# Optimization experiments

Hardware: AMD Instinct MI355X
Metric: run time of the kernel (lower is better)

Reference implementation:

```python
import jax, jax.numpy as jnp
import numpy as np

N_VERTS = 100000
N_FACES = 200000
C = 512


def setup_inputs() -> dict:
    key = jax.random.key(0)
    ks = jax.random.split(key, 12)
    x = jax.random.normal(ks[0], (1, N_VERTS, C), dtype=jnp.float32) * 0.1
    verts = jax.random.normal(ks[1], (N_VERTS, 3), dtype=jnp.float32)
    faces = jax.random.randint(ks[2], (N_FACES, 3), 0, N_VERTS, dtype=jnp.int32)
    def lin(k, fan_in, fan_out):
        return jax.random.normal(k, (fan_in, fan_out), dtype=jnp.float32) / np.sqrt(fan_in)
    return {
        "x": x, "verts": verts, "faces": faces,
        "W1": lin(ks[3], C, C),    "b1": jnp.zeros((C,), jnp.float32),
        "W2": lin(ks[4], C, 512),  "b2": jnp.zeros((512,), jnp.float32),
        "W3": lin(ks[5], 512, 256),"b3": jnp.zeros((256,), jnp.float32),
        "W4": lin(ks[6], 256, 12), "b4": jnp.zeros((12,), jnp.float32),
    }


def special_procrustes(M):
    # roma.special_procrustes: nearest rotation in SO(3) to M, batched [F,3,3]
    U, S, Vh = jnp.linalg.svd(M)
    det = jnp.linalg.det(jnp.matmul(U, Vh))  # [F]
    D = jnp.stack([jnp.ones_like(det), jnp.ones_like(det), det], axis=-1)  # [F,3]
    return jnp.matmul(U * D[:, None, :], Vh)


def reference(x, verts, faces, W1, b1, W2, b2, W3, b3, W4, b4):
    N = verts.shape[0]
    F = faces.shape[0]
    # prism base: gather 3 vertex positions per face -> [F,3,3]
    prism_base = verts[faces]
    # gather features of the 3 face vertices and mean over them -> [F,C]
    feat = x[0][faces].mean(axis=1)
    # mlp_refine
    h = jax.nn.relu(feat @ W1 + b1)
    h = jax.nn.relu(h @ W2 + b2)
    h = jax.nn.relu(h @ W3 + b3)
    out = h @ W4 + b4  # [F,12]
    # batched 3x3 Procrustes rotation + translation
    rotations = special_procrustes(out[:, :9].reshape(F, 3, 3))
    translations = out[:, 9:]  # [F,3]
    transformed_prism = jnp.matmul(prism_base, rotations) + translations[:, None, :]  # [F,3,3]
    # scatter-add back to vertices with per-vertex face-count normalization
    flat_idx = faces.reshape(-1)  # [3F]
    summed = jax.ops.segment_sum(transformed_prism.reshape(-1, 3), flat_idx, num_segments=N)
    counts = jax.ops.segment_sum(jnp.ones((3 * F,), jnp.float32), flat_idx, num_segments=N)
    features = summed / jnp.clip(counts, 1.0)[:, None]  # [N,3]
    return features[None], transformed_prism, rotations
```

## Files before the change

### kernel.cpp

```cpp
#include <hip/hip_runtime.h>
#include <hip/hip_bf16.h>
#include <stdint.h>

typedef __attribute__((ext_vector_type(8))) short short8;
typedef __attribute__((ext_vector_type(4))) float f32x4;
typedef __attribute__((ext_vector_type(4))) unsigned short u16x4;

__device__ __forceinline__ float bf2f(unsigned short h) {
    union { uint32_t u; float f; } v; v.u = ((uint32_t)h) << 16;
    return v.f;
}
__device__ __forceinline__ void split_rne(float f, unsigned short& hi, unsigned short& lo) {
    __hip_bfloat16 h = __float2bfloat16(f);
    union { __hip_bfloat16 b; unsigned short u; } ch; ch.b = h; hi = ch.u;
    float hf = __bfloat162float(h);
    __hip_bfloat16 l = __float2bfloat16(f - hf);
    union { __hip_bfloat16 b; unsigned short u; } cl; cl.b = l; lo = cl.u;
}
__device__ __forceinline__ void splitT(float f, unsigned short& hi, unsigned short& lo) {
    union { float f; uint32_t u; } a; a.f = f;
    hi = (unsigned short)(a.u >> 16);
    union { uint32_t u; float f; } b; b.u = a.u & 0xFFFF0000u;
    union { float f; uint32_t u; } c; c.f = f - b.f;
    lo = (unsigned short)(c.u >> 16);
}

__device__ __forceinline__ void gld_lds16(const void* g, void* s) {
    __builtin_amdgcn_global_load_lds(
        (const __attribute__((address_space(1))) void*)(uintptr_t)g,
        (__attribute__((address_space(3))) void*)(uint32_t)(uintptr_t)s,
        16, 0, 0);
}

__device__ __forceinline__ f32x4 mfma16(short8 a, short8 b, f32x4 c) {
    return __builtin_amdgcn_mfma_f32_16x16x32_bf16(a, b, c, 0, 0, 0);
}

__global__ void prep_weights(const float* __restrict__ W1, const float* __restrict__ W2,
                             const float* __restrict__ W3,
                             unsigned short* __restrict__ w1h, unsigned short* __restrict__ w1l,
                             unsigned short* __restrict__ w2h, unsigned short* __restrict__ w2l,
                             unsigned short* __restrict__ w3h, unsigned short* __restrict__ w3l,
                             float* __restrict__ sums, float* __restrict__ counts, int nverts) {
    int t = blockIdx.x * 256 + threadIdx.x;
    if (t < nverts * 3) sums[t] = 0.0f;
    if (t < nverts)     counts[t] = 0.0f;
    float v; unsigned short *ph, *pl; size_t o;
    if (t < 262144) {
        int k = t >> 9, n = t & 511;
        v = W1[t]; o = (size_t)n * 512 + k; ph = w1h; pl = w1l;
    } else if (t < 524288) {
        int u = t - 262144; int k = u >> 9, n = u & 511;
        v = W2[u]; o = (size_t)n * 512 + k; ph = w2h; pl = w2l;
    } else if (t < 655360) {
        int u = t - 524288; int k = u >> 8, n = u & 255;
        v = W3[u]; o = (size_t)n * 512 + k; ph = w3h; pl = w3l;
    } else return;
    unsigned short hi, lo;
    split_rne(v, hi, lo);
    ph[o] = hi; pl[o] = lo;
}

__global__ void gather_mean(const float* __restrict__ x, const int* __restrict__ faces,
                            unsigned short* __restrict__ Fhi, unsigned short* __restrict__ Flo,
                            int fbase, int fcount, int mrows) {
    int t = blockIdx.x * 256 + threadIdx.x;
    if (t >= (mrows << 7)) return;
    int r = t >> 7;
    int c = (t & 127) << 2;
    f32x4 m = {0.f, 0.f, 0.f, 0.f};
    if (r < fcount) {
        int f = fbase + r;
        int i0 = faces[3 * f], i1 = faces[3 * f + 1], i2 = faces[3 * f + 2];
        f32x4 a = *(const f32x4*)(x + (size_t)i0 * 512 + c);
        f32x4 b = *(const f32x4*)(x + (size_t)i1 * 512 + c);
        f32x4 d = *(const f32x4*)(x + (size_t)i2 * 512 + c);
        m = (a + b + d) * (1.0f / 3.0f);
    }
    u16x4 hv, lv;
#pragma unroll
    for (int j = 0; j < 4; ++j) {
        unsigned short hi, lo;
        split_rne(m[j], hi, lo);
        hv[j] = hi; lv[j] = lo;
    }
    *(u16x4*)(Fhi + (size_t)r * 512 + c) = hv;
    *(u16x4*)(Flo + (size_t)r * 512 + c) = lv;
}

template<int OUT>
__global__ __launch_bounds__(256, 2)
void gemm_pipe(const unsigned short* __restrict__ Ahi, const unsigned short* __restrict__ Alo,
               const unsigned short* __restrict__ Bhi, const unsigned short* __restrict__ Blo,
               const float* __restrict__ bias,
               void* __restrict__ Out0, unsigned short* __restrict__ Olo,
               int N, int K, int nt) {
    __shared__ __align__(16) unsigned short sm[2][4][128 * 32];

    const int tid  = threadIdx.x;
    const int lane = tid & 63;
    const int w    = tid >> 6;
    const int wr = w >> 1, wc = w & 1;

    const int nwg  = gridDim.x;
    const int orig = blockIdx.x;
    const int q = nwg >> 3, r8 = nwg & 7;
    const int xcd = orig & 7, idx = orig >> 3;
    const int wg = (xcd < r8 ? xcd * (q + 1) : r8 * (q + 1) + (xcd - r8) * q) + idx;
    const int m0 = (wg / nt) << 7;
    const int n0 = (wg % nt) << 7;

    f32x4 acc[4][4] = {};

    const int s_lo  = w * 64 + lane;
    const int row0  = s_lo >> 2;
    const int c0    = ((s_lo & 3) - ((row0 >> 1) & 3)) & 3;
    const int s_hi  = 256 + s_lo;
    const int row1  = (s_hi >> 2) & 127;
    const int c1    = ((s_hi & 3) - ((row1 >> 1) & 3)) & 3;

    const uint32_t oA0 = (uint32_t)(m0 + row0) * (uint32_t)K + (c0 << 3);
    const uint32_t oA1 = (uint32_t)(m0 + row1) * (uint32_t)K + (c1 << 3);
    const uint32_t oB0 = (uint32_t)(n0 + row0) * (uint32_t)K + (c0 << 3);
    const uint32_t oB1 = (uint32_t)(n0 + row1) * (uint32_t)K + (c1 << 3);

    auto stage = [&](int b, int t) {
        const uint32_t k0 = t << 5;
        gld_lds16(Ahi + oA0 + k0, &sm[b][0][(w * 64) * 8]);
        gld_lds16(Ahi + oA1 + k0, &sm[b][0][(256 + w * 64) * 8]);
        gld_lds16(Alo + oA0 + k0, &sm[b][1][(w * 64) * 8]);
        gld_lds16(Alo + oA1 + k0, &sm[b][1][(256 + w * 64) * 8]);
        gld_lds16(Bhi + oB0 + k0, &sm[b][2][(w * 64) * 8]);
        gld_lds16(Bhi + oB1 + k0, &sm[b][2][(256 + w * 64) * 8]);
        gld_lds16(Blo + oB0 + k0, &sm[b][3][(w * 64) * 8]);
        gld_lds16(Blo + oB1 + k0, &sm[b][3][(256 + w * 64) * 8]);
    };

    const int NT = K >> 5;
    stage(0, 0);
    stage(1, 1);

    const int kc  = lane >> 4;
    const int rbA = (wr << 6) + (lane & 15);
    const int rbB = (wc << 6) + (lane & 15);

    for (int t = 0; t < NT; ++t) {
        const int cur = t & 1;

        if (t + 1 < NT) asm volatile("s_waitcnt vmcnt(8)" ::: "memory");
        else            asm volatile("s_waitcnt vmcnt(0)" ::: "memory");
        __builtin_amdgcn_s_barrier();

        short8 ah[4], al[4], bh[4], bl[4];
#pragma unroll
        for (int m = 0; m < 4; ++m) {
            const int r   = rbA + (m << 4);
            const int off = r * 32 + (((kc + (r >> 1)) & 3) << 3);
            ah[m] = *(const short8*)&sm[cur][0][off];
            al[m] = *(const short8*)&sm[cur][1][off];
        }
#pragma unroll
        for (int n = 0; n < 4; ++n) {
            const int r   = rbB + (n << 4);
            const int off = r * 32 + (((kc + (r >> 1)) & 3) << 3);
            bh[n] = *(const short8*)&sm[cur][2][off];
            bl[n] = *(const short8*)&sm[cur][3][off];
        }
        asm volatile("s_waitcnt lgkmcnt(0)" ::: "memory");
        __builtin_amdgcn_sched_barrier(0);
        __builtin_amdgcn_s_barrier();

        if (t + 2 < NT) stage(cur, t + 2);

        __builtin_amdgcn_s_setprio(1);
#pragma unroll
        for (int m = 0; m < 4; ++m)
#pragma unroll
            for (int n = 0; n < 4; ++n)
                acc[m][n] = mfma16(ah[m], bh[n], acc[m][n]);
#pragma unroll
        for (int m = 0; m < 4; ++m)
#pragma unroll
            for (int n = 0; n < 4; ++n)
                acc[m][n] = mfma16(al[m], bh[n], acc[m][n]);
#pragma unroll
        for (int m = 0; m < 4; ++m)
#pragma unroll
            for (int n = 0; n < 4; ++n)
                acc[m][n] = mfma16(ah[m], bl[n], acc[m][n]);
        __builtin_amdgcn_s_setprio(0);
    }

#pragma unroll
    for (int n = 0; n < 4; ++n) {
        const int col = n0 + (wc << 6) + (n << 4) + (lane & 15);
        const float bv = (OUT == 1) ? 0.0f : bias[col];
#pragma unroll
        for (int m = 0; m < 4; ++m) {
            const int rbase = m0 + (wr << 6) + (m << 4) + ((lane >> 4) << 2);
#pragma unroll
            for (int j = 0; j < 4; ++j) {
                const size_t o = (size_t)(rbase + j) * N + col;
                if (OUT == 1) {
                    ((float*)Out0)[o] = acc[m][n][j];
                } else if (OUT == 2) {
                    ((float*)Out0)[o] = fmaxf(acc[m][n][j] + bv, 0.0f);
                } else {
                    float v = fmaxf(acc[m][n][j] + bv, 0.0f);
                    unsigned short hi, lo;
                    split_rne(v, hi, lo);
                    ((unsigned short*)Out0)[o] = hi;
                    Olo[o] = lo;
                }
            }
        }
    }
}

__global__ __launch_bounds__(256, 2)
void gemm_l1(const float* __restrict__ X,
             const unsigned short* __restrict__ Bhi, const unsigned short* __restrict__ Blo,
             float* __restrict__ Out,
             int N, int K, int nt, int nvalid) {
    __shared__ __align__(16) unsigned short sm[2][4][128 * 32];

    const int tid  = threadIdx.x;
    const int lane = tid & 63;
    const int w    = tid >> 6;
    const int wr = w >> 1, wc = w & 1;

    const int nwg  = gridDim.x;
    const int orig = blockIdx.x;
    const int q = nwg >> 3, r8 = nwg & 7;
    const int xcd = orig & 7, idx = orig >> 3;
    const int wg = (xcd < r8 ? xcd * (q + 1) : r8 * (q + 1) + (xcd - r8) * q) + idx;
    const int m0 = (wg / nt) << 7;
    const int n0 = (wg % nt) << 7;

    f32x4 acc[4][4] = {};

    int adst[2], avalid[2];
    uint32_t xoff[2];
#pragma unroll
    for (int i = 0; i < 2; ++i) {
        const int s   = i * 256 + tid;
        const int row = s >> 2;
        const int c   = s & 3;
        adst[i]   = row * 32 + (((c + (row >> 1)) & 3) << 3);
        avalid[i] = (m0 + row) < nvalid;
        xoff[i]   = (uint32_t)(avalid[i] ? (m0 + row) : 0) * (uint32_t)K + (c << 3);
    }
    const int s_lo  = w * 64 + lane;
    const int row0  = s_lo >> 2;
    const int c0    = ((s_lo & 3) - ((row0 >> 1) & 3)) & 3;
    const int s_hi  = 256 + s_lo;
    const int row1  = (s_hi >> 2) & 127;
    const int c1    = ((s_hi & 3) - ((row1 >> 1) & 3)) & 3;
    const uint32_t oB0 = (uint32_t)(n0 + row0) * (uint32_t)K + (c0 << 3);
    const uint32_t oB1 = (uint32_t)(n0 + row1) * (uint32_t)K + (c1 << 3);

    f32x4 fA[2][2];

    auto issueA = [&](int t) {
        const uint32_t k0 = t << 5;
#pragma unroll
        for (int i = 0; i < 2; ++i) {
            const float* src = X + xoff[i] + k0;
            fA[i][0] = *(const f32x4*)src;
            fA[i][1] = *(const f32x4*)(src + 4);
        }
    };
    auto issueB = [&](int b, int t) {
        const uint32_t k0 = t << 5;
        gld_lds16(Bhi + oB0 + k0, &sm[b][2][(w * 64) * 8]);
        gld_lds16(Bhi + oB1 + k0, &sm[b][2][(256 + w * 64) * 8]);
        gld_lds16(Blo + oB0 + k0, &sm[b][3][(w * 64) * 8]);
        gld_lds16(Blo + oB1 + k0, &sm[b][3][(256 + w * 64) * 8]);
    };
    auto cvtWriteA = [&](int b) {
#pragma unroll
        for (int i = 0; i < 2; ++i) {
            short8 hv, lv;
#pragma unroll
            for (int j = 0; j < 8; ++j) {
                float f = avalid[i] ? fA[i][j >> 2][j & 3] : 0.0f;
                unsigned short hi, lo;
                splitT(f, hi, lo);
                hv[j] = (short)hi;
                lv[j] = (short)lo;
            }
            *(short8*)&sm[b][0][adst[i]] = hv;
            *(short8*)&sm[b][1][adst[i]] = lv;
        }
    };

    const int NT = K >> 5;
    issueA(0); issueB(0, 0);
    asm volatile("s_waitcnt vmcnt(4)" ::: "memory");
    cvtWriteA(0);
    issueA(1); issueB(1, 1);
    asm volatile("s_waitcnt vmcnt(4)" ::: "memory");
    cvtWriteA(1);
    asm volatile("s_waitcnt lgkmcnt(0)" ::: "memory");

    const int kc  = lane >> 4;
    const int rbA = (wr << 6) + (lane & 15);
    const int rbB = (wc << 6) + (lane & 15);

    for (int t = 0; t < NT; ++t) {
        const int cur = t & 1;

        if (t + 1 < NT) asm volatile("s_waitcnt vmcnt(4)" ::: "memory");
        else            asm volatile("s_waitcnt vmcnt(0)" ::: "memory");
        __builtin_amdgcn_s_barrier();

        if (t + 2 < NT) issueA(t + 2);

        short8 ah[4], al[4], bh[4], bl[4];
#pragma unroll
        for (int m = 0; m < 4; ++m) {
            const int r   = rbA + (m << 4);
            const int off = r * 32 + (((kc + (r >> 1)) & 3) << 3);
            ah[m] = *(const short8*)&sm[cur][0][off];
            al[m] = *(const short8*)&sm[cur][1][off];
        }
#pragma unroll
        for (int n = 0; n < 4; ++n) {
            const int r   = rbB + (n << 4);
            const int off = r * 32 + (((kc + (r >> 1)) & 3) << 3);
            bh[n] = *(const short8*)&sm[cur][2][off];
            bl[n] = *(const short8*)&sm[cur][3][off];
        }
        asm volatile("s_waitcnt lgkmcnt(0)" ::: "memory");
        __builtin_amdgcn_sched_barrier(0);
        __builtin_amdgcn_s_barrier();

        if (t + 2 < NT) issueB(cur, t + 2);

        __builtin_amdgcn_s_setprio(1);
#pragma unroll
        for (int m = 0; m < 4; ++m)
#pragma unroll
            for (int n = 0; n < 4; ++n)
                acc[m][n] = mfma16(ah[m], bh[n], acc[m][n]);
#pragma unroll
        for (int m = 0; m < 4; ++m)
#pragma unroll
            for (int n = 0; n < 4; ++n)
                acc[m][n] = mfma16(al[m], bh[n], acc[m][n]);
#pragma unroll
        for (int m = 0; m < 4; ++m)
#pragma unroll
            for (int n = 0; n < 4; ++n)
                acc[m][n] = mfma16(ah[m], bl[n], acc[m][n]);
        __builtin_amdgcn_s_setprio(0);

        if (t + 2 < NT) {
            asm volatile("s_waitcnt vmcnt(4)" ::: "memory");
            cvtWriteA(cur);
        }
    }

#pragma unroll
    for (int n = 0; n < 4; ++n) {
        const int col = n0 + (wc << 6) + (n << 4) + (lane & 15);
#pragma unroll
        for (int m = 0; m < 4; ++m) {
            const int rbase = m0 + (wr << 6) + (m << 4) + ((lane >> 4) << 2);
#pragma unroll
            for (int j = 0; j < 4; ++j)
                Out[(size_t)(rbase + j) * N + col] = acc[m][n][j];
        }
    }
}

__global__ __launch_bounds__(256, 2)
void gemm_l2w(const float* __restrict__ Y, const int* __restrict__ faces,
              const float* __restrict__ b1,
              const unsigned short* __restrict__ Bhi, const unsigned short* __restrict__ Blo,
              const float* __restrict__ bias2,
              unsigned short* __restrict__ Ohi, unsigned short* __restrict__ Olo,
              int K, int nvalid) {
    __shared__ __align__(16) unsigned short sm[2][2][64 * 32];

    const int tid  = threadIdx.x;
    const int lane = tid & 63;
    const int w    = tid >> 6;

    const int nwg  = gridDim.x;
    const int orig = blockIdx.x;
    const int q = nwg >> 3, r8 = nwg & 7;
    const int xcd = orig & 7, idx = orig >> 3;
    const int wg = (xcd < r8 ? xcd * (q + 1) : r8 * (q + 1) + (xcd - r8) * q) + idx;
    const int m0 = wg << 6;

    f32x4 acc[4][8] = {};

    const int arow = tid >> 2;
    const int achk = tid & 3;
    const int adst = arow * 32 + (((achk + (arow >> 1)) & 3) << 3);
    const int gf   = m0 + arow;
    const int avalid = gf < nvalid;
    const int gfs  = avalid ? gf : 0;
    uint32_t yoff[3];
#pragma unroll
    for (int r = 0; r < 3; ++r)
        yoff[r] = (uint32_t)faces[3 * gfs + r] * (uint32_t)K;

    const uint32_t bBase = (uint32_t)((w << 7) + (lane & 15)) * (uint32_t)K + ((lane >> 4) << 3);

    f32x4 fA[3][2];
    f32x4 fb[2];

    auto issueA = [&](int t) {
        const uint32_t koff = (uint32_t)(t << 5) + (achk << 3);
#pragma unroll
        for (int r = 0; r < 3; ++r) {
            const float* src = Y + yoff[r] + koff;
            fA[r][0] = *(const f32x4*)src;
            fA[r][1] = *(const f32x4*)(src + 4);
        }
        fb[0] = *(const f32x4*)(b1 + koff);
        fb[1] = *(const f32x4*)(b1 + koff + 4);
    };
    auto cvtWriteA = [&](int b) {
        short8 hv, lv;
#pragma unroll
        for (int j = 0; j < 8; ++j) {
            const int h = j >> 2, e = j & 3;
            float f = 0.0f;
            if (avalid) {
                f = fmaf(fA[0][h][e] + fA[1][h][e] + fA[2][h][e], 1.0f / 3.0f, fb[h][e]);
                f = fmaxf(f, 0.0f);
            }
            unsigned short hi, lo;
            splitT(f, hi, lo);
            hv[j] = (short)hi;
            lv[j] = (short)lo;
        }
        *(short8*)&sm[b][0][adst] = hv;
        *(short8*)&sm[b][1][adst] = lv;
    };

    const int NT = K >> 5;
    issueA(0); cvtWriteA(0);
    issueA(1); cvtWriteA(1);
    asm volatile("s_waitcnt lgkmcnt(0)" ::: "memory");
    __builtin_amdgcn_s_barrier();

    const int kc  = lane >> 4;
    const int rlA = lane & 15;

    for (int t = 0; t < NT; ++t) {
        const int cur = t & 1;
        const uint32_t k0 = (uint32_t)(t << 5);

        if (t + 2 < NT) issueA(t + 2);

        short8 bh[4], bl[4];
#pragma unroll
        for (int n = 0; n < 4; ++n) {
            bh[n] = *(const short8*)(Bhi + bBase + (uint32_t)(n * 16) * (uint32_t)K + k0);
            bl[n] = *(const short8*)(Blo + bBase + (uint32_t)(n * 16) * (uint32_t)K + k0);
        }

        short8 ah[4], al[4];
#pragma unroll
        for (int m = 0; m < 4; ++m) {
            const int r   = rlA + (m << 4);
            const int off = r * 32 + (((kc + (r >> 1)) & 3) << 3);
            ah[m] = *(const short8*)&sm[cur][0][off];
            al[m] = *(const short8*)&sm[cur][1][off];
        }
        asm volatile("s_waitcnt lgkmcnt(0)" ::: "memory");
        __builtin_amdgcn_sched_barrier(0);
        __builtin_amdgcn_s_barrier();

        __builtin_amdgcn_s_setprio(1);
#pragma unroll
        for (int m = 0; m < 4; ++m)
#pragma unroll
            for (int n = 0; n < 4; ++n)
                acc[m][n] = mfma16(ah[m], bh[n], acc[m][n]);
#pragma unroll
        for (int m = 0; m < 4; ++m)
#pragma unroll
            for (int n = 0; n < 4; ++n)
                acc[m][n] = mfma16(al[m], bh[n], acc[m][n]);
#pragma unroll
        for (int m = 0; m < 4; ++m)
#pragma unroll
            for (int n = 0; n < 4; ++n)
                acc[m][n] = mfma16(ah[m], bl[n], acc[m][n]);
        __builtin_amdgcn_s_setprio(0);

#pragma unroll
        for (int n = 0; n < 4; ++n) {
            bh[n] = *(const short8*)(Bhi + bBase + (uint32_t)((n + 4) * 16) * (uint32_t)K + k0);
            bl[n] = *(const short8*)(Blo + bBase + (uint32_t)((n + 4) * 16) * (uint32_t)K + k0);
        }
        __builtin_amdgcn_s_setprio(1);
#pragma unroll
        for (int m = 0; m < 4; ++m)
#pragma unroll
            for (int n = 0; n < 4; ++n)
                acc[m][4 + n] = mfma16(ah[m], bh[n], acc[m][4 + n]);
#pragma unroll
        for (int m = 0; m < 4; ++m)
#pragma unroll
            for (int n = 0; n < 4; ++n)
                acc[m][4 + n] = mfma16(al[m], bh[n], acc[m][4 + n]);
#pragma unroll
        for (int m = 0; m < 4; ++m)
#pragma unroll
            for (int n = 0; n < 4; ++n)
                acc[m][4 + n] = mfma16(ah[m], bl[n], acc[m][4 + n]);
        __builtin_amdgcn_s_setprio(0);

        if (t + 2 < NT) cvtWriteA(cur);
    }

#pragma unroll
    for (int n = 0; n < 8; ++n) {
        const int col = (w << 7) + (n << 4) + (lane & 15);
        const float bv = bias2[col];
#pragma unroll
        for (int m = 0; m < 4; ++m) {
            const int rbase = m0 + (m << 4) + ((lane >> 4) << 2);
#pragma unroll
            for (int j = 0; j < 4; ++j) {
                const size_t o = (size_t)(rbase + j) * 512 + col;
                float v = fmaxf(acc[m][n][j] + bv, 0.0f);
                unsigned short hi, lo;
                split_rne(v, hi, lo);
                Ohi[o] = hi;
                Olo[o] = lo;
            }
        }
    }
}

#define JROT(app, aqq, apq, apz, aqz, vp0, vp1, vp2, vq0, vq1, vq2) do {          \
    float _apq = (apq);                                                            \
    if (fabsf(_apq) > 1e-30f) {                                                    \
        float _tau = ((aqq) - (app)) / (2.0f * _apq);                              \
        float _t = copysignf(1.0f, _tau) / (fabsf(_tau) + sqrtf(1.0f + _tau*_tau));\
        float _c = 1.0f / sqrtf(1.0f + _t*_t);                                     \
        float _s = _t * _c;                                                        \
        (app) = (app) - _t * _apq;                                                 \
        (aqq) = (aqq) + _t * _apq;                                                 \
        (apq) = 0.0f;                                                              \
        float _pz = (apz), _qz = (aqz);                                            \
        (apz) = _c * _pz - _s * _qz;                                               \
        (aqz) = _s * _pz + _c * _qz;                                               \
        float _x;                                                                  \
        _x = (vp0); (vp0) = _c*_x - _s*(vq0); (vq0) = _s*_x + _c*(vq0);            \
        _x = (vp1); (vp1) = _c*_x - _s*(vq1); (vq1) = _s*_x + _c*(vq1);            \
        _x = (vp2); (vp2) = _c*_x - _s*(vq2); (vq2) = _s*_x + _c*(vq2);            \
    }                                                                              \
} while (0)

#define SWAP3(la, lb, x0, y0, z0, x1, y1, z1) do {                \
    float _tm;                                                    \
    _tm = la; la = lb; lb = _tm;                                  \
    _tm = x0; x0 = x1; x1 = _tm;                                  \
    _tm = y0; y0 = y1; y1 = _tm;                                  \
    _tm = z0; z0 = z1; z1 = _tm;                                  \
} while (0)

__global__ void face_kernel(const float* __restrict__ H3,
                            const float* __restrict__ W4, const float* __restrict__ b4,
                            const float* __restrict__ verts, const int* __restrict__ faces,
                            float* __restrict__ out_tp, float* __restrict__ out_rot,
                            float* __restrict__ sums, float* __restrict__ counts,
                            int fbase, int fcount) {
    __shared__ float sW[256 * 12 + 12];
    for (int i = threadIdx.x; i < 256 * 12 + 12; i += 256)
        sW[i] = (i < 256 * 12) ? W4[i] : b4[i - 256 * 12];
    __syncthreads();

    const int r = blockIdx.x * 256 + threadIdx.x;
    if (r >= fcount) return;
    const int f = fbase + r;

    float o[12];
#pragma unroll
    for (int n = 0; n < 12; ++n) o[n] = sW[3072 + n];
    const f32x4* ph = (const f32x4*)(H3 + (size_t)r * 256);
    for (int kb = 0; kb < 64; ++kb) {
        f32x4 hv = ph[kb];
#pragma unroll
        for (int kk = 0; kk < 4; ++kk) {
            float val = hv[kk];
            const float* wrow = &sW[(kb * 4 + kk) * 12];
#pragma unroll
            for (int n = 0; n < 12; ++n) o[n] = fmaf(val, wrow[n], o[n]);
        }
    }

    const float M00=o[0], M01=o[1], M02=o[2];
    const float M10=o[3], M11=o[4], M12=o[5];
    const float M20=o[6], M21=o[7], M22=o[8];
    const float t0 =o[9], t1 =o[10], t2 =o[11];

    float a00 = M00*M00 + M10*M10 + M20*M20;
    float a11 = M01*M01 + M11*M11 + M21*M21;
    float a22 = M02*M02 + M12*M12 + M22*M22;
    float a01 = M00*M01 + M10*M11 + M20*M21;
    float a02 = M00*M02 + M10*M12 + M20*M22;
    float a12 = M01*M02 + M11*M12 + M21*M22;

    float v00=1.f, v01=0.f, v02=0.f;
    float v10=0.f, v11=1.f, v12=0.f;
    float v20=0.f, v21=0.f, v22=1.f;
#pragma unroll
    for (int sweep = 0; sweep < 5; ++sweep) {
        JROT(a00, a11, a01, a02, a12, v00, v10, v20, v01, v11, v21);
        JROT(a00, a22, a02, a01, a12, v00, v10, v20, v02, v12, v22);
        JROT(a11, a22, a12, a01, a02, v01, v11, v21, v02, v12, v22);
    }
    float l0 = a00, l1 = a11, l2 = a22;
    if (l0 < l1) SWAP3(l0, l1, v00, v10, v20, v01, v11, v21);
    if (l0 < l2) SWAP3(l0, l2, v00, v10, v20, v02, v12, v22);
    if (l1 < l2) SWAP3(l1, l2, v01, v11, v21, v02, v12, v22);

    float b1x = M00*v00 + M01*v10 + M02*v20;
    float b1y = M10*v00 + M11*v10 + M12*v20;
    float b1z = M20*v00 + M21*v10 + M22*v20;
    float b2x = M00*v01 + M01*v11 + M02*v21;
    float b2y = M10*v01 + M11*v11 + M12*v21;
    float b2z = M20*v01 + M21*v11 + M22*v21;

    float n1 = sqrtf(b1x*b1x + b1y*b1y + b1z*b1z);
    float u1x, u1y, u1z;
    if (n1 > 1e-25f) { float in = 1.0f / n1; u1x = b1x*in; u1y = b1y*in; u1z = b1z*in; }
    else             { u1x = 1.f; u1y = 0.f; u1z = 0.f; }

    float dp  = b2x*u1x + b2y*u1y + b2z*u1z;
    float w2x = b2x - dp*u1x, w2y = b2y - dp*u1y, w2z = b2z - dp*u1z;
    float n2  = sqrtf(w2x*w2x + w2y*w2y + w2z*w2z);
    float u2x, u2y, u2z;
    if (n2 > 1e-25f) { float in = 1.0f / n2; u2x = w2x*in; u2y = w2y*in; u2z = w2z*in; }
    else {
        float ex = (fabsf(u1x) < 0.9f) ? 1.f : 0.f;
        float ey = 1.f - ex;
        float cx = -u1z * ey, cy = u1z * ex, cz = u1x * ey - u1y * ex;
        float cn = rsqrtf(cx*cx + cy*cy + cz*cz);
        u2x = cx * cn; u2y = cy * cn; u2z = cz * cn;
    }
    float u3x = u1y*u2z - u1z*u2y;
    float u3y = u1z*u2x - u1x*u2z;
    float u3z = u1x*u2y - u1y*u2x;

    float dv = v00*(v11*v22 - v12*v21) - v01*(v10*v22 - v12*v20) + v02*(v10*v21 - v11*v20);
    if (dv < 0.f) { v02 = -v02; v12 = -v12; v22 = -v22; }

    float R00 = u1x*v00 + u2x*v01 + u3x*v02;
    float R01 = u1x*v10 + u2x*v11 + u3x*v12;
    float R02 = u1x*v20 + u2x*v21 + u3x*v22;
    float R10 = u1y*v00 + u2y*v01 + u3y*v02;
    float R11 = u1y*v10 + u2y*v11 + u3y*v12;
    float R12 = u1y*v20 + u2y*v21 + u3y*v22;
    float R20 = u1z*v00 + u2z*v01 + u3z*v02;
    float R21 = u1z*v10 + u2z*v11 + u3z*v12;
    float R22 = u1z*v20 + u2z*v21 + u3z*v22;

    float* rp = out_rot + (size_t)f * 9;
    rp[0]=R00; rp[1]=R01; rp[2]=R02;
    rp[3]=R10; rp[4]=R11; rp[5]=R12;
    rp[6]=R20; rp[7]=R21; rp[8]=R22;

    float* tp = out_tp + (size_t)f * 9;
    const int idx[3] = { faces[3*f], faces[3*f+1], faces[3*f+2] };
#pragma unroll
    for (int j = 0; j < 3; ++j) {
        const int vi = idx[j];
        float px = verts[3*vi], py = verts[3*vi+1], pz = verts[3*vi+2];
        float q0 = px*R00 + py*R10 + pz*R20 + t0;
        float q1 = px*R01 + py*R11 + pz*R21 + t1;
        float q2 = px*R02 + py*R12 + pz*R22 + t2;
        tp[j*3+0] = q0; tp[j*3+1] = q1; tp[j*3+2] = q2;
        atomicAdd(&sums[(size_t)vi*3+0], q0);
        atomicAdd(&sums[(size_t)vi*3+1], q1);
        atomicAdd(&sums[(size_t)vi*3+2], q2);
        atomicAdd(&counts[vi], 1.0f);
    }
}

__global__ void finalize_kernel(float* __restrict__ feats, const float* __restrict__ counts, int nverts) {
    int v = blockIdx.x * 256 + threadIdx.x;
    if (v >= nverts) return;
    float c = fmaxf(counts[v], 1.0f);
    feats[v*3+0] = feats[v*3+0] / c;
    feats[v*3+1] = feats[v*3+1] / c;
    feats[v*3+2] = feats[v*3+2] / c;
}

extern "C" void kernel_launch(void* const* d_in, const int* in_sizes, int n_in,
                              void* d_out, int out_size, void* d_ws, size_t ws_size,
                              hipStream_t stream) {
    const float* x     = (const float*)d_in[0];
    const float* verts = (const float*)d_in[1];
    const int*   faces = (const int*)d_in[2];
    const float* W1 = (const float*)d_in[3];
    const float* b1 = (const float*)d_in[4];
    const float* W2 = (const float*)d_in[5];
    const float* b2 = (const float*)d_in[6];
    const float* W3 = (const float*)d_in[7];
    const float* b3 = (const float*)d_in[8];
    const float* W4 = (const float*)d_in[9];
    const float* b4 = (const float*)d_in[10];

    const int nverts = in_sizes[1] / 3;
    const int nfaces = in_sizes[2] / 3;

    float* out_feats = (float*)d_out;
    float* out_tp    = out_feats + (size_t)nverts * 3;
    float* out_rot   = out_tp + (size_t)nfaces * 9;

    char* ws = (char*)d_ws;
    size_t cur = 0;
    auto carve = [&](size_t bytes) -> void* {
        void* p = ws + cur;
        cur += (bytes + 255) & ~(size_t)255;
        return p;
    };
    unsigned short* w1h = (unsigned short*)carve(512 * 512 * 2);
    unsigned short* w1l = (unsigned short*)carve(512 * 512 * 2);
    unsigned short* w2h = (unsigned short*)carve(512 * 512 * 2);
    unsigned short* w2l = (unsigned short*)carve(512 * 512 * 2);
    unsigned short* w3h = (unsigned short*)carve(256 * 512 * 2);
    unsigned short* w3l = (unsigned short*)carve(256 * 512 * 2);
    float* counts = (float*)carve((size_t)nverts * 4);

    const long MV = ((long)nverts + 127) & ~127L;
    const long MF = ((long)nfaces + 127) & ~127L;
    const size_t szY   = (size_t)MV * 512 * 4;
    const size_t szH2w = (size_t)MF * 512 * 2;
    const size_t szH3f = (size_t)MF * 256 * 4;

    const size_t sR1 = (szY > szH3f) ? szY : szH3f;
    const size_t sR2 = szH2w;
    const size_t sR3 = szH2w;
    const size_t need = cur + sR1 + sR2 + sR3 + 4 * 256;

    prep_weights<<<(655360 + 255) / 256, 256, 0, stream>>>(W1, W2, W3, w1h, w1l, w2h, w2l, w3h, w3l,
                                                           out_feats, counts, nverts);

    if (ws_size >= need) {
        char* R1 = (char*)carve(sR1);
        char* R2 = (char*)carve(sR2);
        char* R3 = (char*)carve(sR3);
        float*          y   = (float*)R1;
        float*          h3  = (float*)R1;
        unsigned short* h2h = (unsigned short*)R2;
        unsigned short* h2l = (unsigned short*)R3;

        gemm_l1<<<(int)(MV / 128) * 4, 256, 0, stream>>>(x, w1h, w1l, y, 512, 512, 4, nverts);

        gemm_l2w<<<(int)(MF / 64), 256, 0, stream>>>(y, faces, b1, w2h, w2l, b2,
                                                     h2h, h2l, 512, nfaces);

        gemm_pipe<2><<<(int)(MF / 128) * 2, 256, 0, stream>>>(h2h, h2l, w3h, w3l, b3, h3, nullptr, 256, 512, 2);

        face_kernel<<<(nfaces + 255) / 256, 256, 0, stream>>>(h3, W4, b4, verts, faces,
                                                              out_tp, out_rot, out_feats, counts,
                                                              0, nfaces);
    } else {
        long mpad = MF;
        size_t avail = (ws_size > cur) ? (ws_size - cur) : 0;
        long chp = (long)(avail / 4096);
        chp &= ~127L;
        if (chp > mpad) chp = mpad;
        if (chp < 128) chp = 128;
        unsigned short* bAh = (unsigned short*)carve((size_t)chp * 512 * 2);
        unsigned short* bAl = (unsigned short*)carve((size_t)chp * 512 * 2);
        unsigned short* bBh = (unsigned short*)carve((size_t)chp * 512 * 2);
        unsigned short* bBl = (unsigned short*)carve((size_t)chp * 512 * 2);

        for (long base = 0; base < nfaces; base += chp) {
            long rem = (long)nfaces - base;
            int cnt = (int)((rem < chp) ? rem : chp);
            int mc  = (cnt + 127) & ~127;

            gather_mean<<<mc / 2, 256, 0, stream>>>(x, faces, bAh, bAl, (int)base, cnt, mc);
            gemm_pipe<0><<<(mc / 128) * 4, 256, 0, stream>>>(bAh, bAl, w1h, w1l, b1, bBh, bBl, 512, 512, 4);
            gemm_pipe<0><<<(mc / 128) * 4, 256, 0, stream>>>(bBh, bBl, w2h, w2l, b2, bAh, bAl, 512, 512, 4);
            gemm_pipe<2><<<(mc / 128) * 2, 256, 0, stream>>>(bAh, bAl, w3h, w3l, b3, (float*)bBh, nullptr, 256, 512, 2);
            face_kernel<<<(cnt + 255) / 256, 256, 0, stream>>>((float*)bBh, W4, b4, verts, faces,
                                                               out_tp, out_rot, out_feats, counts,
                                                               (int)base, cnt);
        }
    }

    finalize_kernel<<<(nverts + 255) / 256, 256, 0, stream>>>(out_feats, counts, nverts);
}
```

Measured before the change: 1.182 ms.

## Retile layer-2 gather GEMM to 128x256 tiles with LDS-staged B

Replaces the 64-row, full-width layer-2 GEMM (4 waves, each streaming its B columns directly from global memory) with a 512-thread kernel using 128x256 output tiles across a 2x4 wave grid. The B operand (hi/lo split weights) is now loaded asynchronously into shared memory with swizzled direct-to-LDS loads, so each B fragment is shared across waves instead of being re-read per wave. The A-side gather, mean, bias and ReLU fusion is kept. The change aims to cut redundant global and L2 traffic for the weights and raise MFMA reuse. In exchange the gathered A rows are now loaded twice (once per N half) and there is more barrier synchronization per K step.

```diff
diff --git a/kernel.cpp b/kernel.cpp
--- a/kernel.cpp
+++ b/kernel.cpp
@@ -374,27 +374,30 @@
     }
 }
 
-__global__ __launch_bounds__(256, 2)
-void gemm_l2w(const float* __restrict__ Y, const int* __restrict__ faces,
+__global__ __launch_bounds__(512, 2)
+void gemm_l2n(const float* __restrict__ Y, const int* __restrict__ faces,
               const float* __restrict__ b1,
               const unsigned short* __restrict__ Bhi, const unsigned short* __restrict__ Blo,
               const float* __restrict__ bias2,
               unsigned short* __restrict__ Ohi, unsigned short* __restrict__ Olo,
               int K, int nvalid) {
-    __shared__ __align__(16) unsigned short sm[2][2][64 * 32];
+    __shared__ __align__(16) unsigned short smA[2][2][128 * 32];
+    __shared__ __align__(16) unsigned short smB[2][256 * 32];
 
     const int tid  = threadIdx.x;
     const int lane = tid & 63;
     const int w    = tid >> 6;
+    const int wr = w >> 2, wc = w & 3;
 
     const int nwg  = gridDim.x;
     const int orig = blockIdx.x;
     const int q = nwg >> 3, r8 = nwg & 7;
     const int xcd = orig & 7, idx = orig >> 3;
     const int wg = (xcd < r8 ? xcd * (q + 1) : r8 * (q + 1) + (xcd - r8) * q) + idx;
-    const int m0 = wg << 6;
-
-    f32x4 acc[4][8] = {};
+    const int m0 = (wg >> 1) << 7;
+    const int n0 = (wg & 1) << 8;
+
+    f32x4 acc[4][4] = {};
 
     const int arow = tid >> 2;
     const int achk = tid & 3;
@@ -407,7 +410,12 @@
     for (int r = 0; r < 3; ++r)
         yoff[r] = (uint32_t)faces[3 * gfs + r] * (uint32_t)K;
 
-    const uint32_t bBase = (uint32_t)((w << 7) + (lane & 15)) * (uint32_t)K + ((lane >> 4) << 3);
+    const int brow0 = tid >> 2;
+    const int bc0   = ((tid & 3) - ((brow0 >> 1) & 3)) & 3;
+    const int brow1 = 128 + brow0;
+    const int bc1   = ((tid & 3) - ((brow1 >> 1) & 3)) & 3;
+    const uint32_t oB0 = (uint32_t)(n0 + brow0) * (uint32_t)K + (bc0 << 3);
+    const uint32_t oB1 = (uint32_t)(n0 + brow1) * (uint32_t)K + (bc1 << 3);
 
     f32x4 fA[3][2];
     f32x4 fb[2];
@@ -422,6 +430,13 @@
         }
         fb[0] = *(const f32x4*)(b1 + koff);
         fb[1] = *(const f32x4*)(b1 + koff + 4);
+    };
+    auto issueB = [&](int t) {
+        const uint32_t k0 = t << 5;
+        gld_lds16(Bhi + oB0 + k0, &smB[0][(w * 64) * 8]);
+        gld_lds16(Bhi + oB1 + k0, &smB[0][(512 + w * 64) * 8]);
+        gld_lds16(Blo + oB0 + k0, &smB[1][(w * 64) * 8]);
+        gld_lds16(Blo + oB1 + k0, &smB[1][(512 + w * 64) * 8]);
     };
     auto cvtWriteA = [&](int b) {
         short8 hv, lv;
@@ -438,44 +453,52 @@
             hv[j] = (short)hi;
             lv[j] = (short)lo;
         }
-        *(short8*)&sm[b][0][adst] = hv;
-        *(short8*)&sm[b][1][adst] = lv;
+        *(short8*)&smA[b][0][adst] = hv;
+        *(short8*)&smA[b][1][adst] = lv;
     };
 
     const int NT = K >> 5;
-    issueA(0); cvtWriteA(0);
-    issueA(1); cvtWriteA(1);
+    issueA(0); issueB(0);
+    asm volatile("s_waitcnt vmcnt(4)" ::: "memory");
+    cvtWriteA(0);
+    issueA(1);
+    asm volatile("s_waitcnt vmcnt(0)" ::: "memory");
+    cvtWriteA(1);
     asm volatile("s_waitcnt lgkmcnt(0)" ::: "memory");
-    __builtin_amdgcn_s_barrier();
-
-    const int kc  = lane >> 4;
-    const int rlA = lane & 15;
+
+    const int kc = lane >> 4;
+    const int rA = (wr << 6) + (lane & 15);
+    const int rB = (wc << 6) + (lane & 15);
 
     for (int t = 0; t < NT; ++t) {
         const int cur = t & 1;
-        const uint32_t k0 = (uint32_t)(t << 5);
+
+        asm volatile("s_waitcnt vmcnt(0)" ::: "memory");
+        __builtin_amdgcn_s_barrier();
 
         if (t + 2 < NT) issueA(t + 2);
 
-        short8 bh[4], bl[4];
+        short8 ah[4], al[4], bh[4], bl[4];
+#pragma unroll
+        for (int m = 0; m < 4; ++m) {
+            const int r   = rA + (m << 4);
+            const int off = r * 32 + (((kc + (r >> 1)) & 3) << 3);
+            ah[m] = *(const short8*)&smA[cur][0][off];
+            al[m] = *(const short8*)&smA[cur][1][off];
+        }
 #pragma unroll
         for (int n = 0; n < 4; ++n) {
-            bh[n] = *(const short8*)(Bhi + bBase + (uint32_t)(n * 16) * (uint32_t)K + k0);
-            bl[n] = *(const short8*)(Blo + bBase + (uint32_t)(n * 16) * (uint32_t)K + k0);
-        }
-
-        short8 ah[4], al[4];
-#pragma unroll
-        for (int m = 0; m < 4; ++m) {
-            const int r   = rlA + (m << 4);
+            const int r   = rB + (n << 4);
             const int off = r * 32 + (((kc + (r >> 1)) & 3) << 3);
-            ah[m] = *(const short8*)&sm[cur][0][off];
-            al[m] = *(const short8*)&sm[cur][1][off];
+            bh[n] = *(const short8*)&smB[0][off];
+            bl[n] = *(const short8*)&smB[1][off];
         }
         asm volatile("s_waitcnt lgkmcnt(0)" ::: "memory");
         __builtin_amdgcn_sched_barrier(0);
         __builtin_amdgcn_s_barrier();
 
+        if (t + 1 < NT) issueB(t + 1);
+
         __builtin_amdgcn_s_setprio(1);
 #pragma unroll
         for (int m = 0; m < 4; ++m)
@@ -494,39 +517,19 @@
                 acc[m][n] = mfma16(ah[m], bl[n], acc[m][n]);
         __builtin_amdgcn_s_setprio(0);
 
-#pragma unroll
-        for (int n = 0; n < 4; ++n) {
-            bh[n] = *(const short8*)(Bhi + bBase + (uint32_t)((n + 4) * 16) * (uint32_t)K + k0);
-            bl[n] = *(const short8*)(Blo + bBase + (uint32_t)((n + 4) * 16) * (uint32_t)K + k0);
-        }
-        __builtin_amdgcn_s_setprio(1);
-#pragma unroll
-        for (int m = 0; m < 4; ++m)
-#pragma unroll
-            for (int n = 0; n < 4; ++n)
-                acc[m][4 + n] = mfma16(ah[m], bh[n], acc[m][4 + n]);
-#pragma unroll
-        for (int m = 0; m < 4; ++m)
-#pragma unroll
-            for (int n = 0; n < 4; ++n)
-                acc[m][4 + n] = mfma16(al[m], bh[n], acc[m][4 + n]);
-#pragma unroll
-        for (int m = 0; m < 4; ++m)
-#pragma unroll
-            for (int n = 0; n < 4; ++n)
-                acc[m][4 + n] = mfma16(ah[m], bl[n], acc[m][4 + n]);
-        __builtin_amdgcn_s_setprio(0);
-
-        if (t + 2 < NT) cvtWriteA(cur);
-    }
-
-#pragma unroll
-    for (int n = 0; n < 8; ++n) {
-        const int col = (w << 7) + (n << 4) + (lane & 15);
+        if (t + 2 < NT) {
+            asm volatile("s_waitcnt vmcnt(4)" ::: "memory");
+            cvtWriteA(cur);
+        }
+    }
+
+#pragma unroll
+    for (int n = 0; n < 4; ++n) {
+        const int col = n0 + (wc << 6) + (n << 4) + (lane & 15);
         const float bv = bias2[col];
 #pragma unroll
         for (int m = 0; m < 4; ++m) {
-            const int rbase = m0 + (m << 4) + ((lane >> 4) << 2);
+            const int rbase = m0 + (wr << 6) + (m << 4) + ((lane >> 4) << 2);
 #pragma unroll
             for (int j = 0; j < 4; ++j) {
                 const size_t o = (size_t)(rbase + j) * 512 + col;
@@ -758,8 +761,8 @@
 
         gemm_l1<<<(int)(MV / 128) * 4, 256, 0, stream>>>(x, w1h, w1l, y, 512, 512, 4, nverts);
 
-        gemm_l2w<<<(int)(MF / 64), 256, 0, stream>>>(y, faces, b1, w2h, w2l, b2,
-                                                     h2h, h2l, 512, nfaces);
+        gemm_l2n<<<(int)(MF / 128) * 2, 512, 0, stream>>>(y, faces, b1, w2h, w2l, b2,
+                                                          h2h, h2l, 512, nfaces);
 
         gemm_pipe<2><<<(int)(MF / 128) * 2, 256, 0, stream>>>(h2h, h2l, w3h, w3l, b3, h3, nullptr, 256, 512, 2);
 
```

Result: no change. 1.172 ms (-0.9%).
